# Kernel tuning notes

Measured on AMD Instinct MI355X. Metric: run time of the kernel, lower is better.

The kernel has to match this reference:

```python
import jax, jax.numpy as jnp
import numpy as np

D_MODEL = 1024
NUM_HEADS = 16
D_K = D_MODEL // NUM_HEADS
LOCAL_WINDOW = 256
SCALE = 1.0 / np.float32(np.sqrt(D_K))
NEG = -1e9


def setup_inputs() -> dict:
    key = jax.random.key(0)
    ks = jax.random.split(key, 11)
    B, S, D = 2, 2048, D_MODEL
    s = 1.0 / np.float32(np.sqrt(D))
    return {
        "query": jax.random.normal(ks[0], (B, S, D), jnp.float32),
        "key": jax.random.normal(ks[1], (B, S, D), jnp.float32),
        "value": jax.random.normal(ks[2], (B, S, D), jnp.float32),
        "Wq": jax.random.normal(ks[3], (D, D), jnp.float32) * s,
        "bq": jnp.zeros((D,), jnp.float32),
        "Wk": jax.random.normal(ks[4], (D, D), jnp.float32) * s,
        "bk": jnp.zeros((D,), jnp.float32),
        "Wv": jax.random.normal(ks[5], (D, D), jnp.float32) * s,
        "bv": jnp.zeros((D,), jnp.float32),
        "Wo": jax.random.normal(ks[6], (D, D), jnp.float32) * s,
        "bo": jnp.zeros((D,), jnp.float32),
    }


def _band_mask(S):
    # torch loop: allowed cols j with max(0, i - w//2) <= j < min(S, i + w//2)
    i = jnp.arange(S)
    diff = i[None, :] - i[:, None]  # j - i
    half = LOCAL_WINDOW // 2
    return (diff >= -half) & (diff < half)  # [S, S] bool


def reference(query, key, value, Wq, bq, Wk, bk, Wv, bv, Wo, bo):
    B, S, D = query.shape
    H, dk = NUM_HEADS, D_K

    def proj(x, W, b):
        # nn.Linear: x @ W.T + b ; then split heads -> [B, H, S, dk]
        return (x @ W.T + b).reshape(B, S, H, dk).transpose(0, 2, 1, 3)

    Q = proj(query, Wq, bq)
    K = proj(key, Wk, bk)
    V = proj(value, Wv, bv)

    scores = jnp.einsum("bhqd,bhkd->bhqk", Q, K) * SCALE  # [B,H,S,S]
    band = _band_mask(S)
    scores = jnp.where(band[None, None, :, :], scores, NEG)
    attn = jax.nn.softmax(scores, axis=-1)
    out = jnp.einsum("bhqk,bhkd->bhqd", attn, V)  # [B,H,S,dk]
    out = out.transpose(0, 2, 1, 3).reshape(B, S, D)
    return out @ Wo.T + bo
```

## Files before the change

kernel.cpp:

```cpp
#include <hip/hip_runtime.h>
#include <stdint.h>

#define S_LEN 2048
#define NB 2
#define NH 16
#define DK 64
#define DM 1024
#define QK_SCALE 0.125f
#define NEG_BIG -1e30f

typedef __attribute__((ext_vector_type(8))) short bf16x8;
typedef __attribute__((ext_vector_type(4))) float f32x4;

static __device__ __forceinline__ f32x4 mfma16(bf16x8 a, bf16x8 b, f32x4 c) {
    return __builtin_amdgcn_mfma_f32_16x16x32_bf16(a, b, c, 0, 0, 0);
}

static __device__ __forceinline__ void gload_lds16(const void* g, void* l) {
    __builtin_amdgcn_global_load_lds((const __attribute__((address_space(1))) void*)g,
                                     (__attribute__((address_space(3))) void*)l,
                                     16, 0, 0);
}

static __device__ __forceinline__ unsigned short f2bf(float x) {
    unsigned int u = __float_as_uint(x);
    u += 0x7fffu + ((u >> 16) & 1u);
    return (unsigned short)(u >> 16);
}

struct CvtArgs {
    const float* src[7];
    unsigned short* dst[7];
    int n8[7];
};

__global__ __launch_bounds__(256) void cvt_f32_bf16(CvtArgs a) {
    const int t = blockIdx.y;
    const float* __restrict__ src = a.src[t];
    unsigned short* __restrict__ dst = a.dst[t];
    const int n8 = a.n8[t];
    const int stride = gridDim.x * blockDim.x;
    for (int i = blockIdx.x * blockDim.x + threadIdx.x; i < n8; i += stride) {
        float4 v0 = ((const float4*)src)[(size_t)i * 2];
        float4 v1 = ((const float4*)src)[(size_t)i * 2 + 1];
        union { bf16x8 v; unsigned short h[8]; } u;
        u.h[0] = f2bf(v0.x); u.h[1] = f2bf(v0.y); u.h[2] = f2bf(v0.z); u.h[3] = f2bf(v0.w);
        u.h[4] = f2bf(v1.x); u.h[5] = f2bf(v1.y); u.h[6] = f2bf(v1.z); u.h[7] = f2bf(v1.w);
        ((bf16x8*)dst)[i] = u.v;
    }
}

static __device__ __forceinline__ void gemm_core_128(
    const unsigned short* __restrict__ A,
    const unsigned short* __restrict__ W,
    unsigned short* sA, unsigned short* sB,
    int K, f32x4 acc[4][4])
{
    const int tid = threadIdx.x;
    const int wid = tid >> 6, lane = tid & 63;
    const int m0 = blockIdx.y * 128, n0 = blockIdx.x * 128;
    const int wr = wid >> 1, wc = wid & 1;
    const int fr = lane & 15, fg = lane >> 4;
    const int ldr = lane >> 3, ldc = (lane & 7) * 8;

    const unsigned short* pA = A + (size_t)(m0 + ldr) * K + ldc;
    const unsigned short* pW = W + (size_t)(n0 + ldr) * K + ldc;

    for (int k0 = 0; k0 < K; k0 += 64) {
        __syncthreads();
        #pragma unroll
        for (int it = 0; it < 4; ++it) {
            const int rb = wid * 32 + it * 8;
            gload_lds16(pA + (size_t)(rb)*K + k0, sA + rb * 64);
            gload_lds16(pW + (size_t)(rb)*K + k0, sB + rb * 64);
        }
        __syncthreads();
        #pragma unroll
        for (int kf = 0; kf < 2; ++kf) {
            bf16x8 af[4], bfr[4];
            #pragma unroll
            for (int mf = 0; mf < 4; ++mf)
                af[mf] = *(const bf16x8*)(sA + (wr * 64 + mf * 16 + fr) * 64 + kf * 32 + fg * 8);
            #pragma unroll
            for (int nf = 0; nf < 4; ++nf)
                bfr[nf] = *(const bf16x8*)(sB + (wc * 64 + nf * 16 + fr) * 64 + kf * 32 + fg * 8);
            #pragma unroll
            for (int mf = 0; mf < 4; ++mf)
                #pragma unroll
                for (int nf = 0; nf < 4; ++nf)
                    acc[mf][nf] = mfma16(af[mf], bfr[nf], acc[mf][nf]);
        }
    }
}

__global__ __launch_bounds__(256, 2) void gemm_qkv(
    const unsigned short* __restrict__ Xq, const unsigned short* __restrict__ Xk,
    const unsigned short* __restrict__ Xv,
    const unsigned short* __restrict__ Wq, const unsigned short* __restrict__ Wk,
    const unsigned short* __restrict__ Wv,
    const float* __restrict__ bq, const float* __restrict__ bk, const float* __restrict__ bv,
    unsigned short* __restrict__ Qo, unsigned short* __restrict__ Ko,
    unsigned short* __restrict__ Vt)
{
    __shared__ unsigned short sA[128 * 64];
    __shared__ unsigned short sB[128 * 64];
    const int z = blockIdx.z;
    const unsigned short* A = (z == 0) ? Xq : ((z == 1) ? Xk : Xv);
    const unsigned short* W = (z == 0) ? Wq : ((z == 1) ? Wk : Wv);
    const float* bias = (z == 0) ? bq : ((z == 1) ? bk : bv);

    f32x4 acc[4][4] = {};
    gemm_core_128(A, W, sA, sB, DM, acc);

    const int tid = threadIdx.x, wid = tid >> 6, lane = tid & 63;
    const int m0 = blockIdx.y * 128, n0 = blockIdx.x * 128;
    const int wr = wid >> 1, wc = wid & 1, fr = lane & 15, fg = lane >> 4;
    unsigned short* Oh = (z == 0) ? Qo : Ko;
    #pragma unroll
    for (int nf = 0; nf < 4; ++nf) {
        const int col = n0 + wc * 64 + nf * 16 + fr;
        const float bb = bias[col];
        const int h = col >> 6, dd = col & (DK - 1);
        #pragma unroll
        for (int mf = 0; mf < 4; ++mf) {
            #pragma unroll
            for (int r = 0; r < 4; ++r) {
                const int row = m0 + wr * 64 + mf * 16 + fg * 4 + r;
                const int b = row >> 11, s = row & (S_LEN - 1);
                const float val = acc[mf][nf][r] + bb;
                if (z < 2)
                    Oh[(((size_t)b * NH + h) * S_LEN + s) * DK + dd] = f2bf(val);
                else
                    Vt[(((size_t)b * NH + h) * DK + dd) * S_LEN + s] = f2bf(val);
            }
        }
    }
}

__global__ __launch_bounds__(256, 2) void gemm_out(
    const unsigned short* __restrict__ A, const unsigned short* __restrict__ W,
    const float* __restrict__ bias, float* __restrict__ out)
{
    __shared__ unsigned short sA[128 * 64];
    __shared__ unsigned short sB[128 * 64];
    f32x4 acc[4][4] = {};
    gemm_core_128(A, W, sA, sB, DM, acc);
    const int tid = threadIdx.x, wid = tid >> 6, lane = tid & 63;
    const int m0 = blockIdx.y * 128, n0 = blockIdx.x * 128;
    const int wr = wid >> 1, wc = wid & 1, fr = lane & 15, fg = lane >> 4;
    #pragma unroll
    for (int nf = 0; nf < 4; ++nf) {
        const int col = n0 + wc * 64 + nf * 16 + fr;
        const float bb = bias[col];
        #pragma unroll
        for (int mf = 0; mf < 4; ++mf) {
            #pragma unroll
            for (int r = 0; r < 4; ++r) {
                const int row = m0 + wr * 64 + mf * 16 + fg * 4 + r;
                out[(size_t)row * DM + col] = acc[mf][nf][r] + bb;
            }
        }
    }
}

__global__ __launch_bounds__(256, 2) void attn_kernel(
    const unsigned short* __restrict__ Qb,
    const unsigned short* __restrict__ Kb,
    const unsigned short* __restrict__ Vt,
    unsigned short* __restrict__ Oout)
{
    __shared__ unsigned short sK[128 * 64];
    __shared__ unsigned short sV[64 * 128];
    __shared__ unsigned short sP[4][32 * 128];

    const int tid = threadIdx.x, wid = tid >> 6, lane = tid & 63;
    const int fr = lane & 15, fg = lane >> 4;
    const int qt = blockIdx.x, bh = blockIdx.y;
    const int q0 = qt * 128;
    const size_t base = (size_t)bh * (S_LEN * DK);

    bf16x8 qf[2][2];
    #pragma unroll
    for (int mf = 0; mf < 2; ++mf)
        #pragma unroll
        for (int kf = 0; kf < 2; ++kf)
            qf[mf][kf] = *(const bf16x8*)(Qb + base +
                (size_t)(q0 + wid * 32 + mf * 16 + fr) * DK + kf * 32 + fg * 8);

    f32x4 oacc[2][4] = {};
    float m_run[2][4], l_run[2][4];
    #pragma unroll
    for (int mf = 0; mf < 2; ++mf)
        #pragma unroll
        for (int r = 0; r < 4; ++r) { m_run[mf][r] = NEG_BIG; l_run[mf][r] = 0.f; }

    const int t_lo = (qt == 0) ? 1 : 0;
    const int t_hi = (qt == (S_LEN / 128 - 1)) ? 1 : 2;

    for (int t = t_lo; t <= t_hi; ++t) {
        const int kt0 = q0 + (t - 1) * 128;
        __syncthreads();
        {
            const unsigned short* gK = Kb + base + (size_t)kt0 * DK;
            #pragma unroll
            for (int it = 0; it < 4; ++it) {
                const int chunk = wid * 4 + it;
                gload_lds16(gK + chunk * 512 + lane * 8, sK + chunk * 512);
            }
            const unsigned short* gV = Vt + base + kt0;
            #pragma unroll
            for (int it = 0; it < 4; ++it) {
                const int chunk = wid * 4 + it;
                gload_lds16(gV + (size_t)(chunk * 4 + fg) * S_LEN + fr * 8, sV + chunk * 512);
            }
        }
        __syncthreads();

        f32x4 sacc[2][8] = {};
        #pragma unroll
        for (int kf = 0; kf < 2; ++kf) {
            bf16x8 kfr[8];
            #pragma unroll
            for (int nf = 0; nf < 8; ++nf)
                kfr[nf] = *(const bf16x8*)(sK + (nf * 16 + fr) * 64 + kf * 32 + fg * 8);
            #pragma unroll
            for (int mf = 0; mf < 2; ++mf)
                #pragma unroll
                for (int nf = 0; nf < 8; ++nf)
                    sacc[mf][nf] = mfma16(qf[mf][kf], kfr[nf], sacc[mf][nf]);
        }

        const int dt = (t - 1) * 128;
        #pragma unroll
        for (int mf = 0; mf < 2; ++mf) {
            #pragma unroll
            for (int r = 0; r < 4; ++r) {
                const int row = wid * 32 + mf * 16 + fg * 4 + r;
                float mm = NEG_BIG;
                #pragma unroll
                for (int nf = 0; nf < 8; ++nf) {
                    const int col = nf * 16 + fr;
                    const int diff = dt + col - row;
                    float s = sacc[mf][nf][r] * QK_SCALE;
                    s = (diff >= -128 && diff < 128) ? s : NEG_BIG;
                    sacc[mf][nf][r] = s;
                    mm = fmaxf(mm, s);
                }
                #pragma unroll
                for (int d = 1; d < 16; d <<= 1) mm = fmaxf(mm, __shfl_xor(mm, d));
                const float mold = m_run[mf][r];
                const float mn = fmaxf(mold, mm);
                m_run[mf][r] = mn;
                const float alpha = __expf(mold - mn);
                float ps = 0.f;
                #pragma unroll
                for (int nf = 0; nf < 8; ++nf) {
                    const float p = __expf(sacc[mf][nf][r] - mn);
                    ps += p;
                    sP[wid][(mf * 16 + fg * 4 + r) * 128 + nf * 16 + fr] = f2bf(p);
                }
                #pragma unroll
                for (int d = 1; d < 16; d <<= 1) ps += __shfl_xor(ps, d);
                l_run[mf][r] = l_run[mf][r] * alpha + ps;
                #pragma unroll
                for (int nf = 0; nf < 4; ++nf)
                    oacc[mf][nf][r] = oacc[mf][nf][r] * alpha;
            }
        }

        #pragma unroll
        for (int kf = 0; kf < 4; ++kf) {
            bf16x8 pa[2], vb[4];
            #pragma unroll
            for (int mf = 0; mf < 2; ++mf)
                pa[mf] = *(const bf16x8*)(&sP[wid][(mf * 16 + fr) * 128 + kf * 32 + fg * 8]);
            #pragma unroll
            for (int nf = 0; nf < 4; ++nf)
                vb[nf] = *(const bf16x8*)(sV + (nf * 16 + fr) * 128 + kf * 32 + fg * 8);
            #pragma unroll
            for (int mf = 0; mf < 2; ++mf)
                #pragma unroll
                for (int nf = 0; nf < 4; ++nf)
                    oacc[mf][nf] = mfma16(pa[mf], vb[nf], oacc[mf][nf]);
        }
    }

    const int b = bh >> 4, h = bh & 15;
    #pragma unroll
    for (int mf = 0; mf < 2; ++mf) {
        #pragma unroll
        for (int r = 0; r < 4; ++r) {
            const float inv = 1.0f / l_run[mf][r];
            const int token = b * S_LEN + q0 + wid * 32 + mf * 16 + fg * 4 + r;
            #pragma unroll
            for (int nf = 0; nf < 4; ++nf) {
                const int feat = h * 64 + nf * 16 + fr;
                Oout[(size_t)token * DM + feat] = f2bf(oacc[mf][nf][r] * inv);
            }
        }
    }
}

extern "C" void kernel_launch(void* const* d_in, const int* in_sizes, int n_in,
                              void* d_out, int out_size, void* d_ws, size_t ws_size,
                              hipStream_t stream)
{
    (void)in_sizes; (void)n_in; (void)out_size; (void)ws_size;
    const float* q  = (const float*)d_in[0];
    const float* k  = (const float*)d_in[1];
    const float* v  = (const float*)d_in[2];
    const float* Wq = (const float*)d_in[3];
    const float* bq = (const float*)d_in[4];
    const float* Wk = (const float*)d_in[5];
    const float* bk = (const float*)d_in[6];
    const float* Wv = (const float*)d_in[7];
    const float* bv = (const float*)d_in[8];
    const float* Wo = (const float*)d_in[9];
    const float* bo = (const float*)d_in[10];

    char* ws = (char*)d_ws;
    const size_t MB = 1024 * 1024;
    unsigned short* Xq  = (unsigned short*)(ws + 0 * MB);
    unsigned short* Xk  = (unsigned short*)(ws + 8 * MB);
    unsigned short* Xv  = (unsigned short*)(ws + 16 * MB);
    unsigned short* Qb  = (unsigned short*)(ws + 24 * MB);
    unsigned short* Kb  = (unsigned short*)(ws + 32 * MB);
    unsigned short* Vt  = (unsigned short*)(ws + 40 * MB);
    unsigned short* Wqb = (unsigned short*)(ws + 48 * MB);
    unsigned short* Wkb = (unsigned short*)(ws + 50 * MB);
    unsigned short* Wvb = (unsigned short*)(ws + 52 * MB);
    unsigned short* Wob = (unsigned short*)(ws + 54 * MB);
    unsigned short* AO  = Xq;

    CvtArgs ca;
    ca.src[0] = q;  ca.dst[0] = Xq;  ca.n8[0] = (NB * S_LEN * DM) / 8;
    ca.src[1] = k;  ca.dst[1] = Xk;  ca.n8[1] = (NB * S_LEN * DM) / 8;
    ca.src[2] = v;  ca.dst[2] = Xv;  ca.n8[2] = (NB * S_LEN * DM) / 8;
    ca.src[3] = Wq; ca.dst[3] = Wqb; ca.n8[3] = (DM * DM) / 8;
    ca.src[4] = Wk; ca.dst[4] = Wkb; ca.n8[4] = (DM * DM) / 8;
    ca.src[5] = Wv; ca.dst[5] = Wvb; ca.n8[5] = (DM * DM) / 8;
    ca.src[6] = Wo; ca.dst[6] = Wob; ca.n8[6] = (DM * DM) / 8;
    cvt_f32_bf16<<<dim3(1024, 7), 256, 0, stream>>>(ca);

    gemm_qkv<<<dim3(DM / 128, (NB * S_LEN) / 128, 3), 256, 0, stream>>>(
        Xq, Xk, Xv, Wqb, Wkb, Wvb, bq, bk, bv, Qb, Kb, Vt);

    attn_kernel<<<dim3(S_LEN / 128, NB * NH), 256, 0, stream>>>(Qb, Kb, Vt, AO);

    gemm_out<<<dim3(DM / 128, (NB * S_LEN) / 128), 256, 0, stream>>>(
        AO, Wob, bo, (float*)d_out);
}
```

Measured before the change: 118.0 us.

## Rewrite QKV projection GEMM as 256x256 tile, 8-wave, double-buffered kernel

Replaces the 128x128 four-wave QKV GEMM with a 256x256 tile using 512 threads, an XOR-swizzled LDS layout and double-buffered global-to-LDS prefetch. Compute is interleaved with LDS fragment loads, using s_barrier and setprio to keep the matrix cores busy. The aim is more data reuse per LDS byte, fewer bank conflicts and load latency hidden behind MFMA. The cost is 128KB of LDS per block and only 192 blocks, which may leave CUs underused and limit occupancy; the output GEMM is unchanged apart from a signature refactor.

New measurement: 134.0 us. 1.13x slower.

```diff
diff --git a/kernel.cpp b/kernel.cpp
--- a/kernel.cpp
+++ b/kernel.cpp
@@ -50,50 +50,7 @@
     }
 }
 
-static __device__ __forceinline__ void gemm_core_128(
-    const unsigned short* __restrict__ A,
-    const unsigned short* __restrict__ W,
-    unsigned short* sA, unsigned short* sB,
-    int K, f32x4 acc[4][4])
-{
-    const int tid = threadIdx.x;
-    const int wid = tid >> 6, lane = tid & 63;
-    const int m0 = blockIdx.y * 128, n0 = blockIdx.x * 128;
-    const int wr = wid >> 1, wc = wid & 1;
-    const int fr = lane & 15, fg = lane >> 4;
-    const int ldr = lane >> 3, ldc = (lane & 7) * 8;
-
-    const unsigned short* pA = A + (size_t)(m0 + ldr) * K + ldc;
-    const unsigned short* pW = W + (size_t)(n0 + ldr) * K + ldc;
-
-    for (int k0 = 0; k0 < K; k0 += 64) {
-        __syncthreads();
-        #pragma unroll
-        for (int it = 0; it < 4; ++it) {
-            const int rb = wid * 32 + it * 8;
-            gload_lds16(pA + (size_t)(rb)*K + k0, sA + rb * 64);
-            gload_lds16(pW + (size_t)(rb)*K + k0, sB + rb * 64);
-        }
-        __syncthreads();
-        #pragma unroll
-        for (int kf = 0; kf < 2; ++kf) {
-            bf16x8 af[4], bfr[4];
-            #pragma unroll
-            for (int mf = 0; mf < 4; ++mf)
-                af[mf] = *(const bf16x8*)(sA + (wr * 64 + mf * 16 + fr) * 64 + kf * 32 + fg * 8);
-            #pragma unroll
-            for (int nf = 0; nf < 4; ++nf)
-                bfr[nf] = *(const bf16x8*)(sB + (wc * 64 + nf * 16 + fr) * 64 + kf * 32 + fg * 8);
-            #pragma unroll
-            for (int mf = 0; mf < 4; ++mf)
-                #pragma unroll
-                for (int nf = 0; nf < 4; ++nf)
-                    acc[mf][nf] = mfma16(af[mf], bfr[nf], acc[mf][nf]);
-        }
-    }
-}
-
-__global__ __launch_bounds__(256, 2) void gemm_qkv(
+__global__ __launch_bounds__(512, 2) void gemm_qkv8(
     const unsigned short* __restrict__ Xq, const unsigned short* __restrict__ Xk,
     const unsigned short* __restrict__ Xv,
     const unsigned short* __restrict__ Wq, const unsigned short* __restrict__ Wk,
@@ -102,37 +59,197 @@
     unsigned short* __restrict__ Qo, unsigned short* __restrict__ Ko,
     unsigned short* __restrict__ Vt)
 {
-    __shared__ unsigned short sA[128 * 64];
-    __shared__ unsigned short sB[128 * 64];
+    __shared__ unsigned short lds[65536];
+
+    const int tid = threadIdx.x, wid = tid >> 6, lane = tid & 63;
+    const int wm = wid >> 2, wn = wid & 3;
+    const int fr = lane & 15, fg = lane >> 4;
     const int z = blockIdx.z;
+    const int m0 = blockIdx.y * 256, n0 = blockIdx.x * 256;
+
     const unsigned short* A = (z == 0) ? Xq : ((z == 1) ? Xk : Xv);
     const unsigned short* W = (z == 0) ? Wq : ((z == 1) ? Wk : Wv);
     const float* bias = (z == 0) ? bq : ((z == 1) ? bk : bv);
 
-    f32x4 acc[4][4] = {};
-    gemm_core_128(A, W, sA, sB, DM, acc);
-
-    const int tid = threadIdx.x, wid = tid >> 6, lane = tid & 63;
-    const int m0 = blockIdx.y * 128, n0 = blockIdx.x * 128;
-    const int wr = wid >> 1, wc = wid & 1, fr = lane & 15, fg = lane >> 4;
-    unsigned short* Oh = (z == 0) ? Qo : Ko;
+    const int srow = wid * 8 + (lane >> 3);
+    const int scol = ((lane & 7) ^ (lane >> 3)) * 8;
+    const unsigned short* pA = A + (size_t)(m0 + srow) * DM + scol;
+    const unsigned short* pW = W + (size_t)(n0 + srow) * DM + scol;
+
+    const int base_a = (wm * 128 + fr) * 64;
+    const int base_b = (wn * 64 + fr) * 64;
+    const int ck0 = ((0 * 4 + fg) ^ (fr & 7)) * 8;
+    const int ck1 = ((1 * 4 + fg) ^ (fr & 7)) * 8;
+
+    f32x4 acc[8][4] = {};
+
+    {
+        unsigned short* dA = lds + wid * 512;
+        unsigned short* dB = lds + 16384 + wid * 512;
+        #pragma unroll
+        for (int i = 0; i < 4; ++i) {
+            gload_lds16(pA + (size_t)i * 64 * DM, dA + i * 4096);
+            gload_lds16(pW + (size_t)i * 64 * DM, dB + i * 4096);
+        }
+    }
+    __syncthreads();
+
+    for (int t = 0; t < 16; ++t) {
+        const int c = t & 1;
+        if (t + 1 < 16) {
+            const int k0 = (t + 1) * 64;
+            unsigned short* dA = lds + (c ^ 1) * 32768 + wid * 512;
+            unsigned short* dB = lds + (c ^ 1) * 32768 + 16384 + wid * 512;
+            #pragma unroll
+            for (int i = 0; i < 4; ++i) {
+                gload_lds16(pA + (size_t)i * 64 * DM + k0, dA + i * 4096);
+                gload_lds16(pW + (size_t)i * 64 * DM + k0, dB + i * 4096);
+            }
+        }
+        const unsigned short* sA = lds + c * 32768;
+        const unsigned short* sB = sA + 16384;
+
+        bf16x8 a0, a1, a2, a3, a0k, a1k, a2k, a3k;
+        bf16x8 b0, b1, b2, b3, b0k, b1k, b2k, b3k;
+
+        a0  = *(const bf16x8*)(sA + base_a + 0 * 1024 + ck0);
+        a1  = *(const bf16x8*)(sA + base_a + 1 * 1024 + ck0);
+        a2  = *(const bf16x8*)(sA + base_a + 2 * 1024 + ck0);
+        a3  = *(const bf16x8*)(sA + base_a + 3 * 1024 + ck0);
+        a0k = *(const bf16x8*)(sA + base_a + 0 * 1024 + ck1);
+        a1k = *(const bf16x8*)(sA + base_a + 1 * 1024 + ck1);
+        a2k = *(const bf16x8*)(sA + base_a + 2 * 1024 + ck1);
+        a3k = *(const bf16x8*)(sA + base_a + 3 * 1024 + ck1);
+        b0  = *(const bf16x8*)(sB + base_b + 0 * 1024 + ck0);
+        b1  = *(const bf16x8*)(sB + base_b + 1 * 1024 + ck0);
+        b0k = *(const bf16x8*)(sB + base_b + 0 * 1024 + ck1);
+        b1k = *(const bf16x8*)(sB + base_b + 1 * 1024 + ck1);
+        __builtin_amdgcn_s_barrier();
+        __builtin_amdgcn_s_setprio(1);
+        acc[0][0] = mfma16(a0, b0, acc[0][0]); acc[0][0] = mfma16(a0k, b0k, acc[0][0]);
+        acc[0][1] = mfma16(a0, b1, acc[0][1]); acc[0][1] = mfma16(a0k, b1k, acc[0][1]);
+        acc[1][0] = mfma16(a1, b0, acc[1][0]); acc[1][0] = mfma16(a1k, b0k, acc[1][0]);
+        acc[1][1] = mfma16(a1, b1, acc[1][1]); acc[1][1] = mfma16(a1k, b1k, acc[1][1]);
+        acc[2][0] = mfma16(a2, b0, acc[2][0]); acc[2][0] = mfma16(a2k, b0k, acc[2][0]);
+        acc[2][1] = mfma16(a2, b1, acc[2][1]); acc[2][1] = mfma16(a2k, b1k, acc[2][1]);
+        acc[3][0] = mfma16(a3, b0, acc[3][0]); acc[3][0] = mfma16(a3k, b0k, acc[3][0]);
+        acc[3][1] = mfma16(a3, b1, acc[3][1]); acc[3][1] = mfma16(a3k, b1k, acc[3][1]);
+        __builtin_amdgcn_s_setprio(0);
+        __builtin_amdgcn_s_barrier();
+
+        b2  = *(const bf16x8*)(sB + base_b + 2 * 1024 + ck0);
+        b3  = *(const bf16x8*)(sB + base_b + 3 * 1024 + ck0);
+        b2k = *(const bf16x8*)(sB + base_b + 2 * 1024 + ck1);
+        b3k = *(const bf16x8*)(sB + base_b + 3 * 1024 + ck1);
+        __builtin_amdgcn_s_barrier();
+        __builtin_amdgcn_s_setprio(1);
+        acc[0][2] = mfma16(a0, b2, acc[0][2]); acc[0][2] = mfma16(a0k, b2k, acc[0][2]);
+        acc[0][3] = mfma16(a0, b3, acc[0][3]); acc[0][3] = mfma16(a0k, b3k, acc[0][3]);
+        acc[1][2] = mfma16(a1, b2, acc[1][2]); acc[1][2] = mfma16(a1k, b2k, acc[1][2]);
+        acc[1][3] = mfma16(a1, b3, acc[1][3]); acc[1][3] = mfma16(a1k, b3k, acc[1][3]);
+        acc[2][2] = mfma16(a2, b2, acc[2][2]); acc[2][2] = mfma16(a2k, b2k, acc[2][2]);
+        acc[2][3] = mfma16(a2, b3, acc[2][3]); acc[2][3] = mfma16(a2k, b3k, acc[2][3]);
+        acc[3][2] = mfma16(a3, b2, acc[3][2]); acc[3][2] = mfma16(a3k, b2k, acc[3][2]);
+        acc[3][3] = mfma16(a3, b3, acc[3][3]); acc[3][3] = mfma16(a3k, b3k, acc[3][3]);
+        __builtin_amdgcn_s_setprio(0);
+        __builtin_amdgcn_s_barrier();
+
+        a0  = *(const bf16x8*)(sA + base_a + 4 * 1024 + ck0);
+        a1  = *(const bf16x8*)(sA + base_a + 5 * 1024 + ck0);
+        a2  = *(const bf16x8*)(sA + base_a + 6 * 1024 + ck0);
+        a3  = *(const bf16x8*)(sA + base_a + 7 * 1024 + ck0);
+        a0k = *(const bf16x8*)(sA + base_a + 4 * 1024 + ck1);
+        a1k = *(const bf16x8*)(sA + base_a + 5 * 1024 + ck1);
+        a2k = *(const bf16x8*)(sA + base_a + 6 * 1024 + ck1);
+        a3k = *(const bf16x8*)(sA + base_a + 7 * 1024 + ck1);
+        __builtin_amdgcn_s_barrier();
+        __builtin_amdgcn_s_setprio(1);
+        acc[4][0] = mfma16(a0, b0, acc[4][0]); acc[4][0] = mfma16(a0k, b0k, acc[4][0]);
+        acc[4][1] = mfma16(a0, b1, acc[4][1]); acc[4][1] = mfma16(a0k, b1k, acc[4][1]);
+        acc[5][0] = mfma16(a1, b0, acc[5][0]); acc[5][0] = mfma16(a1k, b0k, acc[5][0]);
+        acc[5][1] = mfma16(a1, b1, acc[5][1]); acc[5][1] = mfma16(a1k, b1k, acc[5][1]);
+        acc[6][0] = mfma16(a2, b0, acc[6][0]); acc[6][0] = mfma16(a2k, b0k, acc[6][0]);
+        acc[6][1] = mfma16(a2, b1, acc[6][1]); acc[6][1] = mfma16(a2k, b1k, acc[6][1]);
+        acc[7][0] = mfma16(a3, b0, acc[7][0]); acc[7][0] = mfma16(a3k, b0k, acc[7][0]);
+        acc[7][1] = mfma16(a3, b1, acc[7][1]); acc[7][1] = mfma16(a3k, b1k, acc[7][1]);
+        __builtin_amdgcn_s_setprio(0);
+        __builtin_amdgcn_s_barrier();
+
+        __builtin_amdgcn_s_setprio(1);
+        acc[4][2] = mfma16(a0, b2, acc[4][2]); acc[4][2] = mfma16(a0k, b2k, acc[4][2]);
+        acc[4][3] = mfma16(a0, b3, acc[4][3]); acc[4][3] = mfma16(a0k, b3k, acc[4][3]);
+        acc[5][2] = mfma16(a1, b2, acc[5][2]); acc[5][2] = mfma16(a1k, b2k, acc[5][2]);
+        acc[5][3] = mfma16(a1, b3, acc[5][3]); acc[5][3] = mfma16(a1k, b3k, acc[5][3]);
+        acc[6][2] = mfma16(a2, b2, acc[6][2]); acc[6][2] = mfma16(a2k, b2k, acc[6][2]);
+        acc[6][3] = mfma16(a2, b3, acc[6][3]); acc[6][3] = mfma16(a2k, b3k, acc[6][3]);
+        acc[7][2] = mfma16(a3, b2, acc[7][2]); acc[7][2] = mfma16(a3k, b2k, acc[7][2]);
+        acc[7][3] = mfma16(a3, b3, acc[7][3]); acc[7][3] = mfma16(a3k, b3k, acc[7][3]);
+        __builtin_amdgcn_s_setprio(0);
+
+        __syncthreads();
+    }
+
+    const unsigned short* Oh = nullptr;  (void)Oh;
+    unsigned short* Ohw = (z == 0) ? Qo : Ko;
     #pragma unroll
     for (int nf = 0; nf < 4; ++nf) {
-        const int col = n0 + wc * 64 + nf * 16 + fr;
+        const int col = n0 + wn * 64 + nf * 16 + fr;
         const float bb = bias[col];
         const int h = col >> 6, dd = col & (DK - 1);
         #pragma unroll
-        for (int mf = 0; mf < 4; ++mf) {
+        for (int mf = 0; mf < 8; ++mf) {
             #pragma unroll
             for (int r = 0; r < 4; ++r) {
-                const int row = m0 + wr * 64 + mf * 16 + fg * 4 + r;
+                const int row = m0 + wm * 128 + mf * 16 + fg * 4 + r;
                 const int b = row >> 11, s = row & (S_LEN - 1);
                 const float val = acc[mf][nf][r] + bb;
                 if (z < 2)
-                    Oh[(((size_t)b * NH + h) * S_LEN + s) * DK + dd] = f2bf(val);
+                    Ohw[(((size_t)b * NH + h) * S_LEN + s) * DK + dd] = f2bf(val);
                 else
                     Vt[(((size_t)b * NH + h) * DK + dd) * S_LEN + s] = f2bf(val);
             }
+        }
+    }
+}
+
+static __device__ __forceinline__ void gemm_core_128(
+    const unsigned short* __restrict__ A,
+    const unsigned short* __restrict__ W,
+    unsigned short* sA, unsigned short* sB,
+    int K, int m0, int n0, f32x4 acc[4][4])
+{
+    const int tid = threadIdx.x;
+    const int wid = tid >> 6, lane = tid & 63;
+    const int wr = wid >> 1, wc = wid & 1;
+    const int fr = lane & 15, fg = lane >> 4;
+    const int ldr = lane >> 3, ldc = (lane & 7) * 8;
+
+    const unsigned short* pA = A + (size_t)(m0 + ldr) * K + ldc;
+    const unsigned short* pW = W + (size_t)(n0 + ldr) * K + ldc;
+
+    for (int k0 = 0; k0 < K; k0 += 64) {
+        __syncthreads();
+        #pragma unroll
+        for (int it = 0; it < 4; ++it) {
+            const int rb = wid * 32 + it * 8;
+            gload_lds16(pA + (size_t)(rb)*K + k0, sA + rb * 64);
+            gload_lds16(pW + (size_t)(rb)*K + k0, sB + rb * 64);
+        }
+        __syncthreads();
+        #pragma unroll
+        for (int kf = 0; kf < 2; ++kf) {
+            bf16x8 af[4], bfr[4];
+            #pragma unroll
+            for (int mf = 0; mf < 4; ++mf)
+                af[mf] = *(const bf16x8*)(sA + (wr * 64 + mf * 16 + fr) * 64 + kf * 32 + fg * 8);
+            #pragma unroll
+            for (int nf = 0; nf < 4; ++nf)
+                bfr[nf] = *(const bf16x8*)(sB + (wc * 64 + nf * 16 + fr) * 64 + kf * 32 + fg * 8);
+            #pragma unroll
+            for (int mf = 0; mf < 4; ++mf)
+                #pragma unroll
+                for (int nf = 0; nf < 4; ++nf)
+                    acc[mf][nf] = mfma16(af[mf], bfr[nf], acc[mf][nf]);
         }
     }
 }
@@ -143,10 +260,10 @@
 {
     __shared__ unsigned short sA[128 * 64];
     __shared__ unsigned short sB[128 * 64];
+    const int m0 = blockIdx.y * 128, n0 = blockIdx.x * 128;
     f32x4 acc[4][4] = {};
-    gemm_core_128(A, W, sA, sB, DM, acc);
+    gemm_core_128(A, W, sA, sB, DM, m0, n0, acc);
     const int tid = threadIdx.x, wid = tid >> 6, lane = tid & 63;
-    const int m0 = blockIdx.y * 128, n0 = blockIdx.x * 128;
     const int wr = wid >> 1, wc = wid & 1, fr = lane & 15, fg = lane >> 4;
     #pragma unroll
     for (int nf = 0; nf < 4; ++nf) {
@@ -342,7 +459,7 @@
     ca.src[6] = Wo; ca.dst[6] = Wob; ca.n8[6] = (DM * DM) / 8;
     cvt_f32_bf16<<<dim3(1024, 7), 256, 0, stream>>>(ca);
 
-    gemm_qkv<<<dim3(DM / 128, (NB * S_LEN) / 128, 3), 256, 0, stream>>>(
+    gemm_qkv8<<<dim3(DM / 256, (NB * S_LEN) / 256, 3), 512, 0, stream>>>(
         Xq, Xk, Xv, Wqb, Wkb, Wvb, bq, bk, bv, Qb, Kb, Vt);
 
     attn_kernel<<<dim3(S_LEN / 128, NB * NH), 256, 0, stream>>>(Qb, Kb, Vt, AO);
```

## Fuse fp32-to-bf16 activation conversion into QKV GEMM A-tile loads

Applied to the files above, without the earlier changes.

The QKV projection GEMM now reads the fp32 activations directly, converts them to bf16 in registers and writes them into an XOR-swizzled LDS tile, so the standalone conversion pass over the three large activation tensors is dropped. The conversion kernel now handles only the four weight matrices, with one element group per thread. This removes a full write and re-read of 24MB of bf16 intermediates. In exchange, each GEMM block reads fp32 A tiles (twice the bytes, re-read once per N-tile), and these go through registers rather than async global-to-LDS loads, which could expose load latency.

New measurement: 144.4 us. 22.3% more time.

```diff
diff --git a/kernel.cpp b/kernel.cpp
--- a/kernel.cpp
+++ b/kernel.cpp
@@ -1,4 +1,5 @@
 #include <hip/hip_runtime.h>
+#include <hip/hip_bf16.h>
 #include <stdint.h>
 
 #define S_LEN 2048
@@ -28,74 +29,34 @@
     return (unsigned short)(u >> 16);
 }
 
+static __device__ __forceinline__ unsigned int pkbf(float lo, float hi) {
+    __hip_bfloat162 h = __float22bfloat162_rn(make_float2(lo, hi));
+    union { __hip_bfloat162 h2; unsigned int w; } u;
+    u.h2 = h;
+    return u.w;
+}
+
 struct CvtArgs {
-    const float* src[7];
-    unsigned short* dst[7];
-    int n8[7];
+    const float* src[4];
+    unsigned short* dst[4];
 };
 
 __global__ __launch_bounds__(256) void cvt_f32_bf16(CvtArgs a) {
     const int t = blockIdx.y;
     const float* __restrict__ src = a.src[t];
     unsigned short* __restrict__ dst = a.dst[t];
-    const int n8 = a.n8[t];
-    const int stride = gridDim.x * blockDim.x;
-    for (int i = blockIdx.x * blockDim.x + threadIdx.x; i < n8; i += stride) {
-        float4 v0 = ((const float4*)src)[(size_t)i * 2];
-        float4 v1 = ((const float4*)src)[(size_t)i * 2 + 1];
-        union { bf16x8 v; unsigned short h[8]; } u;
-        u.h[0] = f2bf(v0.x); u.h[1] = f2bf(v0.y); u.h[2] = f2bf(v0.z); u.h[3] = f2bf(v0.w);
-        u.h[4] = f2bf(v1.x); u.h[5] = f2bf(v1.y); u.h[6] = f2bf(v1.z); u.h[7] = f2bf(v1.w);
-        ((bf16x8*)dst)[i] = u.v;
-    }
-}
-
-static __device__ __forceinline__ void gemm_core_128(
-    const unsigned short* __restrict__ A,
-    const unsigned short* __restrict__ W,
-    unsigned short* sA, unsigned short* sB,
-    int K, f32x4 acc[4][4])
-{
-    const int tid = threadIdx.x;
-    const int wid = tid >> 6, lane = tid & 63;
-    const int m0 = blockIdx.y * 128, n0 = blockIdx.x * 128;
-    const int wr = wid >> 1, wc = wid & 1;
-    const int fr = lane & 15, fg = lane >> 4;
-    const int ldr = lane >> 3, ldc = (lane & 7) * 8;
-
-    const unsigned short* pA = A + (size_t)(m0 + ldr) * K + ldc;
-    const unsigned short* pW = W + (size_t)(n0 + ldr) * K + ldc;
-
-    for (int k0 = 0; k0 < K; k0 += 64) {
-        __syncthreads();
-        #pragma unroll
-        for (int it = 0; it < 4; ++it) {
-            const int rb = wid * 32 + it * 8;
-            gload_lds16(pA + (size_t)(rb)*K + k0, sA + rb * 64);
-            gload_lds16(pW + (size_t)(rb)*K + k0, sB + rb * 64);
-        }
-        __syncthreads();
-        #pragma unroll
-        for (int kf = 0; kf < 2; ++kf) {
-            bf16x8 af[4], bfr[4];
-            #pragma unroll
-            for (int mf = 0; mf < 4; ++mf)
-                af[mf] = *(const bf16x8*)(sA + (wr * 64 + mf * 16 + fr) * 64 + kf * 32 + fg * 8);
-            #pragma unroll
-            for (int nf = 0; nf < 4; ++nf)
-                bfr[nf] = *(const bf16x8*)(sB + (wc * 64 + nf * 16 + fr) * 64 + kf * 32 + fg * 8);
-            #pragma unroll
-            for (int mf = 0; mf < 4; ++mf)
-                #pragma unroll
-                for (int nf = 0; nf < 4; ++nf)
-                    acc[mf][nf] = mfma16(af[mf], bfr[nf], acc[mf][nf]);
-        }
-    }
+    const int i = blockIdx.x * blockDim.x + threadIdx.x;
+    float4 v0 = ((const float4*)src)[(size_t)i * 2];
+    float4 v1 = ((const float4*)src)[(size_t)i * 2 + 1];
+    union { bf16x8 v; unsigned int w[4]; } u;
+    u.w[0] = pkbf(v0.x, v0.y); u.w[1] = pkbf(v0.z, v0.w);
+    u.w[2] = pkbf(v1.x, v1.y); u.w[3] = pkbf(v1.z, v1.w);
+    ((bf16x8*)dst)[i] = u.v;
 }
 
 __global__ __launch_bounds__(256, 2) void gemm_qkv(
-    const unsigned short* __restrict__ Xq, const unsigned short* __restrict__ Xk,
-    const unsigned short* __restrict__ Xv,
+    const float* __restrict__ Xq, const float* __restrict__ Xk,
+    const float* __restrict__ Xv,
     const unsigned short* __restrict__ Wq, const unsigned short* __restrict__ Wk,
     const unsigned short* __restrict__ Wv,
     const float* __restrict__ bq, const float* __restrict__ bk, const float* __restrict__ bv,
@@ -104,17 +65,83 @@
 {
     __shared__ unsigned short sA[128 * 64];
     __shared__ unsigned short sB[128 * 64];
+
+    const int tid = threadIdx.x;
+    const int wid = tid >> 6, lane = tid & 63;
+    const int wr = wid >> 1, wc = wid & 1;
+    const int fr = lane & 15, fg = lane >> 4;
     const int z = blockIdx.z;
-    const unsigned short* A = (z == 0) ? Xq : ((z == 1) ? Xk : Xv);
+    const int m0 = blockIdx.y * 128, n0 = blockIdx.x * 128;
+
+    const float* A = (z == 0) ? Xq : ((z == 1) ? Xk : Xv);
     const unsigned short* W = (z == 0) ? Wq : ((z == 1) ? Wk : Wv);
     const float* bias = (z == 0) ? bq : ((z == 1) ? bk : bv);
 
+    const int ldr = lane >> 3, ldc = (lane & 7) * 8;
+    const unsigned short* pW = W + (size_t)(n0 + ldr) * DM + ldc;
+
+    const int arow = tid >> 1;
+    const int acg0 = (tid & 1) * 4;
+    const float* pA = A + (size_t)(m0 + arow) * DM + acg0 * 8;
+
+    const int cka0 = ((0 + fg) ^ (fr & 7)) * 8;
+    const int cka1 = ((4 + fg) ^ (fr & 7)) * 8;
+
     f32x4 acc[4][4] = {};
-    gemm_core_128(A, W, sA, sB, DM, acc);
-
-    const int tid = threadIdx.x, wid = tid >> 6, lane = tid & 63;
-    const int m0 = blockIdx.y * 128, n0 = blockIdx.x * 128;
-    const int wr = wid >> 1, wc = wid & 1, fr = lane & 15, fg = lane >> 4;
+
+    for (int k0 = 0; k0 < DM; k0 += 64) {
+        __syncthreads();
+        #pragma unroll
+        for (int it = 0; it < 4; ++it) {
+            const int rb = wid * 32 + it * 8;
+            gload_lds16(pW + (size_t)rb * DM + k0, sB + rb * 64);
+        }
+        {
+            const float* ga = pA + k0;
+            float4 f0 = *(const float4*)(ga + 0);
+            float4 f1 = *(const float4*)(ga + 4);
+            float4 f2 = *(const float4*)(ga + 8);
+            float4 f3 = *(const float4*)(ga + 12);
+            float4 f4 = *(const float4*)(ga + 16);
+            float4 f5 = *(const float4*)(ga + 20);
+            float4 f6 = *(const float4*)(ga + 24);
+            float4 f7 = *(const float4*)(ga + 28);
+            union { bf16x8 v; unsigned int w[4]; } u;
+            unsigned short* sArow = sA + arow * 64;
+            const int rsw = arow & 7;
+            u.w[0] = pkbf(f0.x, f0.y); u.w[1] = pkbf(f0.z, f0.w);
+            u.w[2] = pkbf(f1.x, f1.y); u.w[3] = pkbf(f1.z, f1.w);
+            *(bf16x8*)(sArow + ((acg0 + 0) ^ rsw) * 8) = u.v;
+            u.w[0] = pkbf(f2.x, f2.y); u.w[1] = pkbf(f2.z, f2.w);
+            u.w[2] = pkbf(f3.x, f3.y); u.w[3] = pkbf(f3.z, f3.w);
+            *(bf16x8*)(sArow + ((acg0 + 1) ^ rsw) * 8) = u.v;
+            u.w[0] = pkbf(f4.x, f4.y); u.w[1] = pkbf(f4.z, f4.w);
+            u.w[2] = pkbf(f5.x, f5.y); u.w[3] = pkbf(f5.z, f5.w);
+            *(bf16x8*)(sArow + ((acg0 + 2) ^ rsw) * 8) = u.v;
+            u.w[0] = pkbf(f6.x, f6.y); u.w[1] = pkbf(f6.z, f6.w);
+            u.w[2] = pkbf(f7.x, f7.y); u.w[3] = pkbf(f7.z, f7.w);
+            *(bf16x8*)(sArow + ((acg0 + 3) ^ rsw) * 8) = u.v;
+        }
+        __syncthreads();
+
+        #pragma unroll
+        for (int kf = 0; kf < 2; ++kf) {
+            bf16x8 af[4], bfr[4];
+            const int cka = kf ? cka1 : cka0;
+            #pragma unroll
+            for (int mf = 0; mf < 4; ++mf)
+                af[mf] = *(const bf16x8*)(sA + (wr * 64 + mf * 16 + fr) * 64 + cka);
+            #pragma unroll
+            for (int nf = 0; nf < 4; ++nf)
+                bfr[nf] = *(const bf16x8*)(sB + (wc * 64 + nf * 16 + fr) * 64 + kf * 32 + fg * 8);
+            #pragma unroll
+            for (int mf = 0; mf < 4; ++mf)
+                #pragma unroll
+                for (int nf = 0; nf < 4; ++nf)
+                    acc[mf][nf] = mfma16(af[mf], bfr[nf], acc[mf][nf]);
+        }
+    }
+
     unsigned short* Oh = (z == 0) ? Qo : Ko;
     #pragma unroll
     for (int nf = 0; nf < 4; ++nf) {
@@ -137,16 +164,58 @@
     }
 }
 
+static __device__ __forceinline__ void gemm_core_128(
+    const unsigned short* __restrict__ A,
+    const unsigned short* __restrict__ W,
+    unsigned short* sA, unsigned short* sB,
+    int K, int m0, int n0, f32x4 acc[4][4])
+{
+    const int tid = threadIdx.x;
+    const int wid = tid >> 6, lane = tid & 63;
+    const int wr = wid >> 1, wc = wid & 1;
+    const int fr = lane & 15, fg = lane >> 4;
+    const int ldr = lane >> 3, ldc = (lane & 7) * 8;
+
+    const unsigned short* pA = A + (size_t)(m0 + ldr) * K + ldc;
+    const unsigned short* pW = W + (size_t)(n0 + ldr) * K + ldc;
+
+    for (int k0 = 0; k0 < K; k0 += 64) {
+        __syncthreads();
+        #pragma unroll
+        for (int it = 0; it < 4; ++it) {
+            const int rb = wid * 32 + it * 8;
+            gload_lds16(pA + (size_t)(rb)*K + k0, sA + rb * 64);
+            gload_lds16(pW + (size_t)(rb)*K + k0, sB + rb * 64);
+        }
+        __syncthreads();
+        #pragma unroll
+        for (int kf = 0; kf < 2; ++kf) {
+            bf16x8 af[4], bfr[4];
+            #pragma unroll
+            for (int mf = 0; mf < 4; ++mf)
+                af[mf] = *(const bf16x8*)(sA + (wr * 64 + mf * 16 + fr) * 64 + kf * 32 + fg * 8);
+            #pragma unroll
+            for (int nf = 0; nf < 4; ++nf)
+                bfr[nf] = *(const bf16x8*)(sB + (wc * 64 + nf * 16 + fr) * 64 + kf * 32 + fg * 8);
+            #pragma unroll
+            for (int mf = 0; mf < 4; ++mf)
+                #pragma unroll
+                for (int nf = 0; nf < 4; ++nf)
+                    acc[mf][nf] = mfma16(af[mf], bfr[nf], acc[mf][nf]);
+        }
+    }
+}
+
 __global__ __launch_bounds__(256, 2) void gemm_out(
     const unsigned short* __restrict__ A, const unsigned short* __restrict__ W,
     const float* __restrict__ bias, float* __restrict__ out)
 {
     __shared__ unsigned short sA[128 * 64];
     __shared__ unsigned short sB[128 * 64];
+    const int m0 = blockIdx.y * 128, n0 = blockIdx.x * 128;
     f32x4 acc[4][4] = {};
-    gemm_core_128(A, W, sA, sB, DM, acc);
+    gemm_core_128(A, W, sA, sB, DM, m0, n0, acc);
     const int tid = threadIdx.x, wid = tid >> 6, lane = tid & 63;
-    const int m0 = blockIdx.y * 128, n0 = blockIdx.x * 128;
     const int wr = wid >> 1, wc = wid & 1, fr = lane & 15, fg = lane >> 4;
     #pragma unroll
     for (int nf = 0; nf < 4; ++nf) {
@@ -320,30 +389,24 @@
 
     char* ws = (char*)d_ws;
     const size_t MB = 1024 * 1024;
-    unsigned short* Xq  = (unsigned short*)(ws + 0 * MB);
-    unsigned short* Xk  = (unsigned short*)(ws + 8 * MB);
-    unsigned short* Xv  = (unsigned short*)(ws + 16 * MB);
-    unsigned short* Qb  = (unsigned short*)(ws + 24 * MB);
-    unsigned short* Kb  = (unsigned short*)(ws + 32 * MB);
-    unsigned short* Vt  = (unsigned short*)(ws + 40 * MB);
-    unsigned short* Wqb = (unsigned short*)(ws + 48 * MB);
-    unsigned short* Wkb = (unsigned short*)(ws + 50 * MB);
-    unsigned short* Wvb = (unsigned short*)(ws + 52 * MB);
-    unsigned short* Wob = (unsigned short*)(ws + 54 * MB);
-    unsigned short* AO  = Xq;
+    unsigned short* AO  = (unsigned short*)(ws + 0 * MB);
+    unsigned short* Qb  = (unsigned short*)(ws + 8 * MB);
+    unsigned short* Kb  = (unsigned short*)(ws + 16 * MB);
+    unsigned short* Vt  = (unsigned short*)(ws + 24 * MB);
+    unsigned short* Wqb = (unsigned short*)(ws + 32 * MB);
+    unsigned short* Wkb = (unsigned short*)(ws + 34 * MB);
+    unsigned short* Wvb = (unsigned short*)(ws + 36 * MB);
+    unsigned short* Wob = (unsigned short*)(ws + 38 * MB);
 
     CvtArgs ca;
-    ca.src[0] = q;  ca.dst[0] = Xq;  ca.n8[0] = (NB * S_LEN * DM) / 8;
-    ca.src[1] = k;  ca.dst[1] = Xk;  ca.n8[1] = (NB * S_LEN * DM) / 8;
-    ca.src[2] = v;  ca.dst[2] = Xv;  ca.n8[2] = (NB * S_LEN * DM) / 8;
-    ca.src[3] = Wq; ca.dst[3] = Wqb; ca.n8[3] = (DM * DM) / 8;
-    ca.src[4] = Wk; ca.dst[4] = Wkb; ca.n8[4] = (DM * DM) / 8;
-    ca.src[5] = Wv; ca.dst[5] = Wvb; ca.n8[5] = (DM * DM) / 8;
-    ca.src[6] = Wo; ca.dst[6] = Wob; ca.n8[6] = (DM * DM) / 8;
-    cvt_f32_bf16<<<dim3(1024, 7), 256, 0, stream>>>(ca);
+    ca.src[0] = Wq; ca.dst[0] = Wqb;
+    ca.src[1] = Wk; ca.dst[1] = Wkb;
+    ca.src[2] = Wv; ca.dst[2] = Wvb;
+    ca.src[3] = Wo; ca.dst[3] = Wob;
+    cvt_f32_bf16<<<dim3((DM * DM / 8) / 256, 4), 256, 0, stream>>>(ca);
 
     gemm_qkv<<<dim3(DM / 128, (NB * S_LEN) / 128, 3), 256, 0, stream>>>(
-        Xq, Xk, Xv, Wqb, Wkb, Wvb, bq, bk, bv, Qb, Kb, Vt);
+        q, k, v, Wqb, Wkb, Wvb, bq, bk, bv, Qb, Kb, Vt);
 
     attn_kernel<<<dim3(S_LEN / 128, NB * NH), 256, 0, stream>>>(Qb, Kb, Vt, AO);
 
```
